# Kernel optimization log

Measured on AMD Instinct MI355X. Metric: run time of the kernel, lower is better.

Reference implementation:

```python
import jax, jax.numpy as jnp
import numpy as np

D_MODEL = 1024
NHEAD = 16
HEAD_DIM = D_MODEL // NHEAD


def setup_inputs() -> dict:
    key = jax.random.key(0)
    ks = jax.random.split(key, 11)
    B, S, D = 4, 2048, D_MODEL
    scale = 1.0 / np.sqrt(D)
    inp = {
        'q': jax.random.normal(ks[0], (B, S, D), jnp.float32),
        'k': jax.random.normal(ks[1], (B, S, D), jnp.float32),
        'v': jax.random.normal(ks[2], (B, S, D), jnp.float32),
        'Wq': jax.random.normal(ks[3], (D, D), jnp.float32) * scale,
        'bq': jnp.zeros((D,), jnp.float32),
        'Wk': jax.random.normal(ks[4], (D, D), jnp.float32) * scale,
        'bk': jnp.zeros((D,), jnp.float32),
        'Wv': jax.random.normal(ks[5], (D, D), jnp.float32) * scale,
        'bv': jnp.zeros((D,), jnp.float32),
        'Wo': jax.random.normal(ks[6], (D, D), jnp.float32) * scale,
        'bo': jnp.zeros((D,), jnp.float32),
    }
    return inp


def reference(q, k, v, Wq, bq, Wk, bk, Wv, bv, Wo, bo):
    B, S, D = q.shape
    H, Hd = NHEAD, HEAD_DIM
    # projections (torch Linear: x @ W.T + b), then split heads -> [B,H,S,Hd]
    qh = (q @ Wq.T + bq).reshape(B, S, H, Hd).transpose(0, 2, 1, 3)
    kh = (k @ Wk.T + bk).reshape(B, S, H, Hd).transpose(0, 2, 1, 3)
    vh = (v @ Wv.T + bv).reshape(B, S, H, Hd).transpose(0, 2, 1, 3)
    # scaled dot-product attention (mask=None, dropout eval-mode identity)
    scores = jnp.einsum('bhqd,bhkd->bhqk', qh, kh) / jnp.sqrt(jnp.float32(Hd))
    attn = jax.nn.softmax(scores, axis=-1)
    out = jnp.einsum('bhqk,bhkd->bhqd', attn, vh)  # [B,H,S,Hd]
    out = out.transpose(0, 2, 1, 3).reshape(B, S, D)
    return out @ Wo.T + bo
```

## Files before the change

### kernel.cpp

```cpp
#include <hip/hip_runtime.h>
#include <cstdint>

using u16 = unsigned short;
using u32 = unsigned int;
typedef __bf16 bf16x8 __attribute__((ext_vector_type(8)));
typedef float f32x4 __attribute__((ext_vector_type(4)));
typedef float f32x16 __attribute__((ext_vector_type(16)));
typedef u16 u16x8 __attribute__((ext_vector_type(8)));
typedef u16 u16x4 __attribute__((ext_vector_type(4)));

#define DEV static __device__ __forceinline__

DEV u16 f2bf(float f) {
  uint32_t u = __builtin_bit_cast(uint32_t, f);
  u += 0x7FFFu + ((u >> 16) & 1u);
  return (u16)(u >> 16);
}
DEV float bf2f(u16 h) {
  uint32_t u = ((uint32_t)h) << 16;
  return __builtin_bit_cast(float, u);
}
DEV u32 cvt_pk_bf16(float lo, float hi) {
  u32 r;
  asm("v_cvt_pk_bf16_f32 %0, %1, %2" : "=v"(r) : "v"(lo), "v"(hi));
  return r;
}

typedef const u32 __attribute__((address_space(1))) gcu32;
typedef u32 __attribute__((address_space(3))) lu32;
DEV void gl_lds16(const u16* g, u16* l) {
  __builtin_amdgcn_global_load_lds((gcu32*)g, (lu32*)l, 16, 0, 0);
}

#define MFMA(a, b, c) __builtin_amdgcn_mfma_f32_16x16x32_bf16((a), (b), (c), 0, 0, 0)
#define MFMA32(a, b, c) __builtin_amdgcn_mfma_f32_32x32x16_bf16((a), (b), (c), 0, 0, 0)

#define WAITV(n) asm volatile("s_waitcnt vmcnt(" #n ")" ::: "memory")

__global__ __launch_bounds__(256) void cvt_all(
    const float* __restrict__ q, const float* __restrict__ k,
    const float* __restrict__ v, const float* __restrict__ Wq,
    const float* __restrict__ Wk, const float* __restrict__ Wv,
    const float* __restrict__ Wo, u16* __restrict__ Xb, u16* __restrict__ Wb,
    u16* __restrict__ WoB) {
  const int bid = blockIdx.x;
  const float* src;
  u16* dst;
  size_t i;
  if (bid < 12288) {
    const int z = bid >> 12;
    src = (z == 0) ? q : (z == 1) ? k : v;
    dst = Xb + (size_t)z * 8388608;
    i = ((size_t)(bid & 4095) * 256 + threadIdx.x) * 8;
  } else {
    const int r = bid - 12288;
    const int z = r >> 9;
    src = (z == 0) ? Wq : (z == 1) ? Wk : (z == 2) ? Wv : Wo;
    dst = (z < 3) ? (Wb + (size_t)z * 1048576) : WoB;
    i = ((size_t)(r & 511) * 256 + threadIdx.x) * 8;
  }
  const float4 a = *(const float4*)(src + i);
  const float4 b = *(const float4*)(src + i + 4);
  u16x8 o;
  o[0] = f2bf(a.x); o[1] = f2bf(a.y); o[2] = f2bf(a.z); o[3] = f2bf(a.w);
  o[4] = f2bf(b.x); o[5] = f2bf(b.y); o[6] = f2bf(b.z); o[7] = f2bf(b.w);
  *(u16x8*)(dst + i) = o;
}

__global__ __launch_bounds__(256) void proj_gemm_bf(
    const u16* __restrict__ Xb, const u16* __restrict__ Wb,
    const float* __restrict__ bq, const float* __restrict__ bk,
    const float* __restrict__ bv, u16* __restrict__ Qh, u16* __restrict__ Kh,
    u16* __restrict__ Vt) {
  __shared__ u16 As[2][128 * 64];
  __shared__ u16 Bs[2][128 * 64];
  const int z = blockIdx.z;
  const int m0 = blockIdx.x * 128, n0 = blockIdx.y * 128;

  const u16* x = Xb + (size_t)z * 8388608;
  const u16* W = Wb + (size_t)z * 1048576;
  const float* bias = (z == 0) ? bq : (z == 1) ? bk : bv;
  u16* out = (z == 0) ? Qh : (z == 1) ? Kh : Vt;
  const float oscale = (z == 0) ? 0.18033688011112042f : 1.0f;

  const int tid = threadIdx.x;
  const int w = tid >> 6, lane = tid & 63;
  const int wr = w >> 1, wc = w & 1;
  const int lr = lane & 15, hq = lane >> 4;

  const int srow = w * 8 + (lane >> 3);
  const int scol = ((lane & 7) ^ ((lane >> 3) & 7)) * 8;
  const u16* xg = x + (size_t)(m0 + srow) * 1024 + scol;
  const u16* wg_ = W + (size_t)(n0 + srow) * 1024 + scol;

  f32x4 acc[4][4];
  const f32x4 fzero = {0.f, 0.f, 0.f, 0.f};
#pragma unroll
  for (int m = 0; m < 4; ++m)
#pragma unroll
    for (int n = 0; n < 4; ++n) acc[m][n] = fzero;

#define PSTAGE(b, t)                                                          \
  {                                                                           \
    _Pragma("unroll") for (int c = 0; c < 4; ++c) {                           \
      gl_lds16(xg + (size_t)c * 32 * 1024 + (t) * 64,                         \
               &As[b][c * 2048 + w * 512]);                                   \
      gl_lds16(wg_ + (size_t)c * 32 * 1024 + (t) * 64,                        \
               &Bs[b][c * 2048 + w * 512]);                                   \
    }                                                                         \
  }

  PSTAGE(0, 0);

#pragma unroll
  for (int t = 0; t < 16; ++t) {
    const int cur = t & 1;
    if (t < 15) {
      PSTAGE(cur ^ 1, t + 1);
      WAITV(8);
    } else {
      WAITV(0);
    }
    __builtin_amdgcn_s_barrier();
    __builtin_amdgcn_sched_barrier(0);
    __builtin_amdgcn_s_setprio(1);
#pragma unroll
    for (int kk = 0; kk < 2; ++kk) {
      bf16x8 a[4], b[4];
#pragma unroll
      for (int m = 0; m < 4; ++m) {
        const int row = wr * 64 + m * 16 + lr;
        a[m] = *(const bf16x8*)&As[cur][row * 64 + (((kk * 4 + hq) ^ (lr & 7)) * 8)];
      }
#pragma unroll
      for (int n = 0; n < 4; ++n) {
        const int row = wc * 64 + n * 16 + lr;
        b[n] = *(const bf16x8*)&Bs[cur][row * 64 + (((kk * 4 + hq) ^ (lr & 7)) * 8)];
      }
#pragma unroll
      for (int m = 0; m < 4; ++m)
#pragma unroll
        for (int n = 0; n < 4; ++n) acc[m][n] = MFMA(a[m], b[n], acc[m][n]);
    }
    __builtin_amdgcn_s_setprio(0);
    __builtin_amdgcn_sched_barrier(0);
    __builtin_amdgcn_s_barrier();
  }
#undef PSTAGE

#pragma unroll
  for (int n = 0; n < 4; ++n) {
    const int col = n0 + wc * 64 + n * 16 + lr;
    const float bvv = bias[col];
    const int h = col >> 6, d = col & 63;
#pragma unroll
    for (int m = 0; m < 4; ++m) {
#pragma unroll
      for (int j = 0; j < 4; ++j) {
        const int rowg = m0 + wr * 64 + m * 16 + hq * 4 + j;
        const int bb = rowg >> 11, s = rowg & 2047;
        const float val = (acc[m][n][j] + bvv) * oscale;
        size_t idx;
        if (z != 2)
          idx = ((size_t)(bb * 16 + h) * 2048 + s) * 64 + d;
        else
          idx = ((size_t)(bb * 16 + h) * 64 + d) * 2048 + s;
        out[idx] = f2bf(val);
      }
    }
  }
}

__global__ __launch_bounds__(256) void proj_gemm_f32(
    const float* __restrict__ q, const float* __restrict__ k,
    const float* __restrict__ v, const float* __restrict__ Wq,
    const float* __restrict__ Wk, const float* __restrict__ Wv,
    const float* __restrict__ bq, const float* __restrict__ bk,
    const float* __restrict__ bv, u16* __restrict__ Qh, u16* __restrict__ Kh,
    u16* __restrict__ Vt) {
  __shared__ u16 As[128][40];
  __shared__ u16 Bs[128][40];
  const int z = blockIdx.z;
  const float* x = (z == 0) ? q : (z == 1) ? k : v;
  const float* W = (z == 0) ? Wq : (z == 1) ? Wk : Wv;
  const float* bias = (z == 0) ? bq : (z == 1) ? bk : bv;
  u16* out = (z == 0) ? Qh : (z == 1) ? Kh : Vt;
  const float oscale = (z == 0) ? 0.18033688011112042f : 1.0f;

  const int tid = threadIdx.x;
  const int m0 = blockIdx.y * 128, n0 = blockIdx.x * 128;
  const int w = tid >> 6, lane = tid & 63;
  const int wr = w >> 1, wc = w & 1;
  const int lr = lane & 15, lk = (lane >> 4) * 8;
  const int srow = tid >> 3, sc4 = (tid & 7) * 4;

  f32x4 acc[4][4];
  const f32x4 fzero = {0.f, 0.f, 0.f, 0.f};
#pragma unroll
  for (int m = 0; m < 4; ++m)
#pragma unroll
    for (int n = 0; n < 4; ++n) acc[m][n] = fzero;

  for (int kt = 0; kt < 32; ++kt) {
    const int k0 = kt * 32;
    __syncthreads();
#pragma unroll
    for (int c = 0; c < 4; ++c) {
      const float4 av = *(const float4*)(x + (size_t)(m0 + c * 32 + srow) * 1024 + k0 + sc4);
      const float4 bvv = *(const float4*)(W + (size_t)(n0 + c * 32 + srow) * 1024 + k0 + sc4);
      u16x4 ah, bh;
      ah[0] = f2bf(av.x); ah[1] = f2bf(av.y); ah[2] = f2bf(av.z); ah[3] = f2bf(av.w);
      bh[0] = f2bf(bvv.x); bh[1] = f2bf(bvv.y); bh[2] = f2bf(bvv.z); bh[3] = f2bf(bvv.w);
      *(u16x4*)&As[c * 32 + srow][sc4] = ah;
      *(u16x4*)&Bs[c * 32 + srow][sc4] = bh;
    }
    __syncthreads();
    bf16x8 a[4], b[4];
#pragma unroll
    for (int m = 0; m < 4; ++m)
      a[m] = *(const bf16x8*)&As[wr * 64 + m * 16 + lr][lk];
#pragma unroll
    for (int n = 0; n < 4; ++n)
      b[n] = *(const bf16x8*)&Bs[wc * 64 + n * 16 + lr][lk];
#pragma unroll
    for (int m = 0; m < 4; ++m)
#pragma unroll
      for (int n = 0; n < 4; ++n) acc[m][n] = MFMA(a[m], b[n], acc[m][n]);
  }

#pragma unroll
  for (int n = 0; n < 4; ++n) {
    const int col = n0 + wc * 64 + n * 16 + lr;
    const float bvv = bias[col];
    const int h = col >> 6, d = col & 63;
#pragma unroll
    for (int m = 0; m < 4; ++m) {
#pragma unroll
      for (int j = 0; j < 4; ++j) {
        const int rowg = m0 + wr * 64 + m * 16 + (lane >> 4) * 4 + j;
        const int bb = rowg >> 11, s = rowg & 2047;
        const float val = (acc[m][n][j] + bvv) * oscale;
        size_t idx;
        if (z != 2)
          idx = ((size_t)(bb * 16 + h) * 2048 + s) * 64 + d;
        else
          idx = ((size_t)(bb * 16 + h) * 64 + d) * 2048 + s;
        out[idx] = f2bf(val);
      }
    }
  }
}

__global__ __launch_bounds__(512, 4) void attn_fwd(
    const u16* __restrict__ Qh, const u16* __restrict__ Kh,
    const u16* __restrict__ Vt, u16* __restrict__ Att) {
  __shared__ u16 Ks[128][72];
  __shared__ u16 Vs[64][136];
  const int tid = threadIdx.x;
  const int w = tid >> 6, lane = tid & 63;
  const int lq = lane & 31, h = lane >> 5;
  const int head = blockIdx.x, q0 = blockIdx.y * 256;
  const u16* Qb = Qh + (size_t)head * 131072;
  const u16* Kb = Kh + (size_t)head * 131072;
  const u16* Vb = Vt + (size_t)head * 131072;
  const int qrow = q0 + w * 32 + lq;

  bf16x8 qf[4];
#pragma unroll
  for (int dc = 0; dc < 4; ++dc)
    qf[dc] = *(const bf16x8*)(Qb + (size_t)qrow * 64 + dc * 16 + h * 8);

  f32x16 o0 = {}, o1 = {};
  float lsum = 0.f;

  const int srow = tid >> 3, scol = (tid & 7) * 8;
  uint4 kr0, kr1, vr0, vr1;
  kr0 = *(const uint4*)(Kb + (size_t)srow * 64 + scol);
  kr1 = *(const uint4*)(Kb + (size_t)(64 + srow) * 64 + scol);
  vr0 = *(const uint4*)(Vb + (size_t)srow * 2048 + scol);
  vr1 = *(const uint4*)(Vb + (size_t)srow * 2048 + 64 + scol);

  for (int kt = 0; kt < 16; ++kt) {
    __syncthreads();
    *(uint4*)&Ks[srow][scol] = kr0;
    *(uint4*)&Ks[64 + srow][scol] = kr1;
    *(uint4*)&Vs[srow][scol] = vr0;
    *(uint4*)&Vs[srow][64 + scol] = vr1;
    __syncthreads();
    if (kt + 1 < 16) {
      const int t0n = (kt + 1) * 128;
      kr0 = *(const uint4*)(Kb + (size_t)(t0n + srow) * 64 + scol);
      kr1 = *(const uint4*)(Kb + (size_t)(t0n + 64 + srow) * 64 + scol);
      vr0 = *(const uint4*)(Vb + (size_t)srow * 2048 + t0n + scol);
      vr1 = *(const uint4*)(Vb + (size_t)srow * 2048 + t0n + 64 + scol);
    }

#pragma unroll
    for (int half = 0; half < 2; ++half) {
      const int ko = half * 64;

      f32x16 s0 = {}, s1 = {};
      __builtin_amdgcn_s_setprio(1);
#pragma unroll
      for (int dc = 0; dc < 4; ++dc) {
        const bf16x8 k0 = *(const bf16x8*)&Ks[ko + lq][dc * 16 + h * 8];
        const bf16x8 k1 = *(const bf16x8*)&Ks[ko + 32 + lq][dc * 16 + h * 8];
        s0 = MFMA32(k0, qf[dc], s0);
        s1 = MFMA32(k1, qf[dc], s1);
      }
      __builtin_amdgcn_s_setprio(0);

      float rs = 0.f;
#pragma unroll
      for (int r = 0; r < 16; ++r) {
        s0[r] = __builtin_amdgcn_exp2f(s0[r]);
        s1[r] = __builtin_amdgcn_exp2f(s1[r]);
        rs += s0[r];
        rs += s1[r];
      }
      lsum += rs;

      u32 w0[8], w1[8];
#pragma unroll
      for (int b = 0; b < 4; ++b)
#pragma unroll
        for (int e = 0; e < 2; ++e) {
          w0[b * 2 + e] = cvt_pk_bf16(s0[4 * b + 2 * e], s0[4 * b + 2 * e + 1]);
          w1[b * 2 + e] = cvt_pk_bf16(s1[4 * b + 2 * e], s1[4 * b + 2 * e + 1]);
        }

      bf16x8 pa[4];
#pragma unroll
      for (int c = 0; c < 2; ++c) {
        u32 a0 = w0[(2 * c) * 2 + 0], b0 = w0[(2 * c + 1) * 2 + 0];
        u32 a1 = w0[(2 * c) * 2 + 1], b1 = w0[(2 * c + 1) * 2 + 1];
        asm("v_permlane32_swap_b32 %0, %1" : "+v"(a0), "+v"(b0));
        asm("v_permlane32_swap_b32 %0, %1" : "+v"(a1), "+v"(b1));
        const uint4 f = {a0, a1, b0, b1};
        pa[c] = __builtin_bit_cast(bf16x8, f);
      }
#pragma unroll
      for (int c = 0; c < 2; ++c) {
        u32 a0 = w1[(2 * c) * 2 + 0], b0 = w1[(2 * c + 1) * 2 + 0];
        u32 a1 = w1[(2 * c) * 2 + 1], b1 = w1[(2 * c + 1) * 2 + 1];
        asm("v_permlane32_swap_b32 %0, %1" : "+v"(a0), "+v"(b0));
        asm("v_permlane32_swap_b32 %0, %1" : "+v"(a1), "+v"(b1));
        const uint4 f = {a0, a1, b0, b1};
        pa[2 + c] = __builtin_bit_cast(bf16x8, f);
      }

      __builtin_amdgcn_s_setprio(1);
#pragma unroll
      for (int c = 0; c < 4; ++c) {
        const bf16x8 v0f = *(const bf16x8*)&Vs[lq][ko + c * 16 + h * 8];
        const bf16x8 v1f = *(const bf16x8*)&Vs[32 + lq][ko + c * 16 + h * 8];
        o0 = MFMA32(pa[c], v0f, o0);
        o1 = MFMA32(pa[c], v1f, o1);
      }
      __builtin_amdgcn_s_setprio(0);
    }
  }

  lsum += __shfl_xor(lsum, 32);

  const int bb = head >> 4, hh = head & 15;
  const float linv = 1.0f / lsum;
#pragma unroll
  for (int r = 0; r < 16; ++r) {
    const int qr = (r & 3) + 8 * (r >> 2) + 4 * h;
    const float li = __shfl(linv, qr);
    const int qg = q0 + w * 32 + qr;
    const size_t base = ((size_t)(bb * 2048 + qg)) * 1024 + hh * 64;
    Att[base + lq] = f2bf(o0[r] * li);
    Att[base + 32 + lq] = f2bf(o1[r] * li);
  }
}

__global__ __launch_bounds__(256) void out_gemm_bf(
    const u16* __restrict__ Att, const u16* __restrict__ WoB,
    const float* __restrict__ bo, float* __restrict__ out) {
  __shared__ u16 As[2][128 * 64];
  __shared__ u16 Bs[2][128 * 64];
  const int m0 = blockIdx.x * 128, n0 = blockIdx.y * 128;
  const int tid = threadIdx.x;
  const int w = tid >> 6, lane = tid & 63;
  const int wr = w >> 1, wc = w & 1;
  const int lr = lane & 15, hq = lane >> 4;

  const int srow = w * 8 + (lane >> 3);
  const int scol = ((lane & 7) ^ ((lane >> 3) & 7)) * 8;
  const u16* ag = Att + (size_t)(m0 + srow) * 1024 + scol;
  const u16* bg = WoB + (size_t)(n0 + srow) * 1024 + scol;

  f32x4 acc[4][4];
  const f32x4 fzero = {0.f, 0.f, 0.f, 0.f};
#pragma unroll
  for (int m = 0; m < 4; ++m)
#pragma unroll
    for (int n = 0; n < 4; ++n) acc[m][n] = fzero;

#define OSTAGE(b, t)                                                          \
  {                                                                           \
    _Pragma("unroll") for (int c = 0; c < 4; ++c) {                           \
      gl_lds16(ag + (size_t)c * 32 * 1024 + (t) * 64,                         \
               &As[b][c * 2048 + w * 512]);                                   \
      gl_lds16(bg + (size_t)c * 32 * 1024 + (t) * 64,                         \
               &Bs[b][c * 2048 + w * 512]);                                   \
    }                                                                         \
  }

  OSTAGE(0, 0);

#pragma unroll
  for (int t = 0; t < 16; ++t) {
    const int cur = t & 1;
    if (t < 15) {
      OSTAGE(cur ^ 1, t + 1);
      WAITV(8);
    } else {
      WAITV(0);
    }
    __builtin_amdgcn_s_barrier();
    __builtin_amdgcn_sched_barrier(0);
    __builtin_amdgcn_s_setprio(1);
#pragma unroll
    for (int kk = 0; kk < 2; ++kk) {
      bf16x8 a[4], b[4];
#pragma unroll
      for (int m = 0; m < 4; ++m) {
        const int row = wr * 64 + m * 16 + lr;
        a[m] = *(const bf16x8*)&As[cur][row * 64 + (((kk * 4 + hq) ^ (lr & 7)) * 8)];
      }
#pragma unroll
      for (int n = 0; n < 4; ++n) {
        const int row = wc * 64 + n * 16 + lr;
        b[n] = *(const bf16x8*)&Bs[cur][row * 64 + (((kk * 4 + hq) ^ (lr & 7)) * 8)];
      }
#pragma unroll
      for (int m = 0; m < 4; ++m)
#pragma unroll
        for (int n = 0; n < 4; ++n) acc[m][n] = MFMA(a[m], b[n], acc[m][n]);
    }
    __builtin_amdgcn_s_setprio(0);
    __builtin_amdgcn_sched_barrier(0);
    __builtin_amdgcn_s_barrier();
  }
#undef OSTAGE

#pragma unroll
  for (int n = 0; n < 4; ++n) {
    const int col = n0 + wc * 64 + n * 16 + lr;
    const float bvv = bo[col];
#pragma unroll
    for (int m = 0; m < 4; ++m)
#pragma unroll
      for (int j = 0; j < 4; ++j) {
        const int rowg = m0 + wr * 64 + m * 16 + hq * 4 + j;
        out[(size_t)rowg * 1024 + col] = acc[m][n][j] + bvv;
      }
  }
}

__global__ __launch_bounds__(256) void out_gemm_f32(
    const u16* __restrict__ Att, const float* __restrict__ Wo,
    const float* __restrict__ bo, float* __restrict__ out) {
  __shared__ u16 As[128][40], Bs[128][40];
  const int tid = threadIdx.x;
  const int m0 = blockIdx.y * 128, n0 = blockIdx.x * 128;
  const int w = tid >> 6, lane = tid & 63;
  const int wr = w >> 1, wc = w & 1;
  const int lr = lane & 15, lk = (lane >> 4) * 8;
  const int arow = tid >> 2, ac8 = (tid & 3) * 8;
  const int wrow = tid >> 3, wc4 = (tid & 7) * 4;

  f32x4 acc[4][4];
  const f32x4 fzero = {0.f, 0.f, 0.f, 0.f};
#pragma unroll
  for (int m = 0; m < 4; ++m)
#pragma unroll
    for (int n = 0; n < 4; ++n) acc[m][n] = fzero;

  for (int kt = 0; kt < 32; ++kt) {
    const int k0 = kt * 32;
    __syncthreads();
#pragma unroll
    for (int c = 0; c < 2; ++c) {
      *(uint4*)&As[c * 64 + arow][ac8] =
          *(const uint4*)(Att + (size_t)(m0 + c * 64 + arow) * 1024 + k0 + ac8);
    }
#pragma unroll
    for (int c = 0; c < 4; ++c) {
      const float4 wv = *(const float4*)(Wo + (size_t)(n0 + c * 32 + wrow) * 1024 + k0 + wc4);
      u16x4 hv;
      hv[0] = f2bf(wv.x); hv[1] = f2bf(wv.y); hv[2] = f2bf(wv.z); hv[3] = f2bf(wv.w);
      *(u16x4*)&Bs[c * 32 + wrow][wc4] = hv;
    }
    __syncthreads();
    bf16x8 a[4], b[4];
#pragma unroll
    for (int m = 0; m < 4; ++m)
      a[m] = *(const bf16x8*)&As[wr * 64 + m * 16 + lr][lk];
#pragma unroll
    for (int n = 0; n < 4; ++n)
      b[n] = *(const bf16x8*)&Bs[wc * 64 + n * 16 + lr][lk];
#pragma unroll
    for (int m = 0; m < 4; ++m)
#pragma unroll
      for (int n = 0; n < 4; ++n) acc[m][n] = MFMA(a[m], b[n], acc[m][n]);
  }

#pragma unroll
  for (int n = 0; n < 4; ++n) {
    const int col = n0 + wc * 64 + n * 16 + lr;
    const float bvv = bo[col];
#pragma unroll
    for (int m = 0; m < 4; ++m)
#pragma unroll
      for (int j = 0; j < 4; ++j) {
        const int rowg = m0 + wr * 64 + m * 16 + (lane >> 4) * 4 + j;
        out[(size_t)rowg * 1024 + col] = acc[m][n][j] + bvv;
      }
  }
}

extern "C" void kernel_launch(void* const* d_in, const int* in_sizes, int n_in,
                              void* d_out, int out_size, void* d_ws, size_t ws_size,
                              hipStream_t stream) {
  const float* q  = (const float*)d_in[0];
  const float* k  = (const float*)d_in[1];
  const float* v  = (const float*)d_in[2];
  const float* Wq = (const float*)d_in[3];
  const float* bq = (const float*)d_in[4];
  const float* Wk = (const float*)d_in[5];
  const float* bk = (const float*)d_in[6];
  const float* Wv = (const float*)d_in[7];
  const float* bv = (const float*)d_in[8];
  const float* Wo = (const float*)d_in[9];
  const float* bo = (const float*)d_in[10];

  u16* ws  = (u16*)d_ws;
  u16* Qh  = ws;
  u16* Kh  = ws + (size_t)8388608;
  u16* Vt  = ws + (size_t)16777216;
  u16* Att = ws + (size_t)25165824;
  u16* Xb  = ws + (size_t)25165824;
  u16* Wb  = ws + (size_t)50331648;
  u16* WoB = ws + (size_t)53477376;
  const size_t need = (size_t)55574528 * 2;

  if (ws_size >= need) {
    cvt_all<<<dim3(14336), dim3(256), 0, stream>>>(q, k, v, Wq, Wk, Wv, Wo, Xb,
                                                   Wb, WoB);
    proj_gemm_bf<<<dim3(64, 8, 3), dim3(256), 0, stream>>>(Xb, Wb, bq, bk, bv,
                                                           Qh, Kh, Vt);
    attn_fwd<<<dim3(64, 8), dim3(512), 0, stream>>>(Qh, Kh, Vt, Att);
    out_gemm_bf<<<dim3(64, 8), dim3(256), 0, stream>>>(Att, WoB, bo,
                                                       (float*)d_out);
  } else {
    proj_gemm_f32<<<dim3(8, 64, 3), dim3(256), 0, stream>>>(
        q, k, v, Wq, Wk, Wv, bq, bk, bv, Qh, Kh, Vt);
    attn_fwd<<<dim3(64, 8), dim3(512), 0, stream>>>(Qh, Kh, Vt, Att);
    out_gemm_f32<<<dim3(8, 64), dim3(256), 0, stream>>>(Att, Wo, bo,
                                                        (float*)d_out);
  }
}
```

Before: 191.3 us.

## Widen bf16 GEMM tiles to 128x256 with 8 waves and triple-buffered LDS

```diff
diff --git a/kernel.cpp b/kernel.cpp
--- a/kernel.cpp
+++ b/kernel.cpp
@@ -67,15 +67,15 @@
   *(u16x8*)(dst + i) = o;
 }
 
-__global__ __launch_bounds__(256) void proj_gemm_bf(
+__global__ __launch_bounds__(512, 2) void proj_gemm_bf(
     const u16* __restrict__ Xb, const u16* __restrict__ Wb,
     const float* __restrict__ bq, const float* __restrict__ bk,
     const float* __restrict__ bv, u16* __restrict__ Qh, u16* __restrict__ Kh,
     u16* __restrict__ Vt) {
-  __shared__ u16 As[2][128 * 64];
-  __shared__ u16 Bs[2][128 * 64];
+  __shared__ u16 As[3][128 * 64];
+  __shared__ u16 Bs[3][256 * 64];
   const int z = blockIdx.z;
-  const int m0 = blockIdx.x * 128, n0 = blockIdx.y * 128;
+  const int m0 = blockIdx.x * 128, n0 = blockIdx.y * 256;
 
   const u16* x = Xb + (size_t)z * 8388608;
   const u16* W = Wb + (size_t)z * 1048576;
@@ -85,13 +85,12 @@
 
   const int tid = threadIdx.x;
   const int w = tid >> 6, lane = tid & 63;
-  const int wr = w >> 1, wc = w & 1;
+  const int wr = w >> 2, wc = w & 3;
   const int lr = lane & 15, hq = lane >> 4;
 
-  const int srow = w * 8 + (lane >> 3);
   const int scol = ((lane & 7) ^ ((lane >> 3) & 7)) * 8;
-  const u16* xg = x + (size_t)(m0 + srow) * 1024 + scol;
-  const u16* wg_ = W + (size_t)(n0 + srow) * 1024 + scol;
+  const u16* xg = x + (size_t)(m0 + w * 8 + (lane >> 3)) * 1024 + scol;
+  const u16* wg_ = W + (size_t)(n0 + w * 8 + (lane >> 3)) * 1024 + scol;
 
   f32x4 acc[4][4];
   const f32x4 fzero = {0.f, 0.f, 0.f, 0.f};
@@ -102,22 +101,25 @@
 
 #define PSTAGE(b, t)                                                          \
   {                                                                           \
-    _Pragma("unroll") for (int c = 0; c < 4; ++c) {                           \
-      gl_lds16(xg + (size_t)c * 32 * 1024 + (t) * 64,                         \
-               &As[b][c * 2048 + w * 512]);                                   \
-      gl_lds16(wg_ + (size_t)c * 32 * 1024 + (t) * 64,                        \
-               &Bs[b][c * 2048 + w * 512]);                                   \
-    }                                                                         \
+    _Pragma("unroll") for (int l = 0; l < 2; ++l)                             \
+      gl_lds16(xg + (size_t)l * 64 * 1024 + (t) * 64,                         \
+               &As[b][(l * 512 + w * 64) * 8]);                               \
+    _Pragma("unroll") for (int l = 0; l < 4; ++l)                             \
+      gl_lds16(wg_ + (size_t)l * 64 * 1024 + (t) * 64,                        \
+               &Bs[b][(l * 512 + w * 64) * 8]);                               \
   }
 
   PSTAGE(0, 0);
+  PSTAGE(1, 1);
 
 #pragma unroll
   for (int t = 0; t < 16; ++t) {
-    const int cur = t & 1;
-    if (t < 15) {
-      PSTAGE(cur ^ 1, t + 1);
-      WAITV(8);
+    const int cur = t % 3;
+    if (t < 14) {
+      PSTAGE((t + 2) % 3, t + 2);
+      WAITV(12);
+    } else if (t == 14) {
+      WAITV(6);
     } else {
       WAITV(0);
     }
@@ -126,16 +128,17 @@
     __builtin_amdgcn_s_setprio(1);
 #pragma unroll
     for (int kk = 0; kk < 2; ++kk) {
+      const int rchunk = ((kk * 4 + hq) ^ (lr & 7)) * 8;
       bf16x8 a[4], b[4];
 #pragma unroll
       for (int m = 0; m < 4; ++m) {
         const int row = wr * 64 + m * 16 + lr;
-        a[m] = *(const bf16x8*)&As[cur][row * 64 + (((kk * 4 + hq) ^ (lr & 7)) * 8)];
+        a[m] = *(const bf16x8*)&As[cur][row * 64 + rchunk];
       }
 #pragma unroll
       for (int n = 0; n < 4; ++n) {
         const int row = wc * 64 + n * 16 + lr;
-        b[n] = *(const bf16x8*)&Bs[cur][row * 64 + (((kk * 4 + hq) ^ (lr & 7)) * 8)];
+        b[n] = *(const bf16x8*)&Bs[cur][row * 64 + rchunk];
       }
 #pragma unroll
       for (int m = 0; m < 4; ++m)
@@ -376,21 +379,20 @@
   }
 }
 
-__global__ __launch_bounds__(256) void out_gemm_bf(
+__global__ __launch_bounds__(512, 2) void out_gemm_bf(
     const u16* __restrict__ Att, const u16* __restrict__ WoB,
     const float* __restrict__ bo, float* __restrict__ out) {
-  __shared__ u16 As[2][128 * 64];
-  __shared__ u16 Bs[2][128 * 64];
-  const int m0 = blockIdx.x * 128, n0 = blockIdx.y * 128;
+  __shared__ u16 As[3][128 * 64];
+  __shared__ u16 Bs[3][256 * 64];
+  const int m0 = blockIdx.x * 128, n0 = blockIdx.y * 256;
   const int tid = threadIdx.x;
   const int w = tid >> 6, lane = tid & 63;
-  const int wr = w >> 1, wc = w & 1;
+  const int wr = w >> 2, wc = w & 3;
   const int lr = lane & 15, hq = lane >> 4;
 
-  const int srow = w * 8 + (lane >> 3);
   const int scol = ((lane & 7) ^ ((lane >> 3) & 7)) * 8;
-  const u16* ag = Att + (size_t)(m0 + srow) * 1024 + scol;
-  const u16* bg = WoB + (size_t)(n0 + srow) * 1024 + scol;
+  const u16* ag = Att + (size_t)(m0 + w * 8 + (lane >> 3)) * 1024 + scol;
+  const u16* bg = WoB + (size_t)(n0 + w * 8 + (lane >> 3)) * 1024 + scol;
 
   f32x4 acc[4][4];
   const f32x4 fzero = {0.f, 0.f, 0.f, 0.f};
@@ -401,22 +403,25 @@
 
 #define OSTAGE(b, t)                                                          \
   {                                                                           \
-    _Pragma("unroll") for (int c = 0; c < 4; ++c) {                           \
-      gl_lds16(ag + (size_t)c * 32 * 1024 + (t) * 64,                         \
-               &As[b][c * 2048 + w * 512]);                                   \
-      gl_lds16(bg + (size_t)c * 32 * 1024 + (t) * 64,                         \
-               &Bs[b][c * 2048 + w * 512]);                                   \
-    }                                                                         \
+    _Pragma("unroll") for (int l = 0; l < 2; ++l)                             \
+      gl_lds16(ag + (size_t)l * 64 * 1024 + (t) * 64,                         \
+               &As[b][(l * 512 + w * 64) * 8]);                               \
+    _Pragma("unroll") for (int l = 0; l < 4; ++l)                             \
+      gl_lds16(bg + (size_t)l * 64 * 1024 + (t) * 64,                         \
+               &Bs[b][(l * 512 + w * 64) * 8]);                               \
   }
 
   OSTAGE(0, 0);
+  OSTAGE(1, 1);
 
 #pragma unroll
   for (int t = 0; t < 16; ++t) {
-    const int cur = t & 1;
-    if (t < 15) {
-      OSTAGE(cur ^ 1, t + 1);
-      WAITV(8);
+    const int cur = t % 3;
+    if (t < 14) {
+      OSTAGE((t + 2) % 3, t + 2);
+      WAITV(12);
+    } else if (t == 14) {
+      WAITV(6);
     } else {
       WAITV(0);
     }
@@ -425,16 +430,17 @@
     __builtin_amdgcn_s_setprio(1);
 #pragma unroll
     for (int kk = 0; kk < 2; ++kk) {
+      const int rchunk = ((kk * 4 + hq) ^ (lr & 7)) * 8;
       bf16x8 a[4], b[4];
 #pragma unroll
       for (int m = 0; m < 4; ++m) {
         const int row = wr * 64 + m * 16 + lr;
-        a[m] = *(const bf16x8*)&As[cur][row * 64 + (((kk * 4 + hq) ^ (lr & 7)) * 8)];
+        a[m] = *(const bf16x8*)&As[cur][row * 64 + rchunk];
       }
 #pragma unroll
       for (int n = 0; n < 4; ++n) {
         const int row = wc * 64 + n * 16 + lr;
-        b[n] = *(const bf16x8*)&Bs[cur][row * 64 + (((kk * 4 + hq) ^ (lr & 7)) * 8)];
+        b[n] = *(const bf16x8*)&Bs[cur][row * 64 + rchunk];
       }
 #pragma unroll
       for (int m = 0; m < 4; ++m)
@@ -551,10 +557,10 @@
   if (ws_size >= need) {
     cvt_all<<<dim3(14336), dim3(256), 0, stream>>>(q, k, v, Wq, Wk, Wv, Wo, Xb,
                                                    Wb, WoB);
-    proj_gemm_bf<<<dim3(64, 8, 3), dim3(256), 0, stream>>>(Xb, Wb, bq, bk, bv,
+    proj_gemm_bf<<<dim3(64, 4, 3), dim3(512), 0, stream>>>(Xb, Wb, bq, bk, bv,
                                                            Qh, Kh, Vt);
     attn_fwd<<<dim3(64, 8), dim3(512), 0, stream>>>(Qh, Kh, Vt, Att);
-    out_gemm_bf<<<dim3(64, 8), dim3(256), 0, stream>>>(Att, WoB, bo,
+    out_gemm_bf<<<dim3(64, 4), dim3(512), 0, stream>>>(Att, WoB, bo,
                                                        (float*)d_out);
   } else {
     proj_gemm_f32<<<dim3(8, 64, 3), dim3(256), 0, stream>>>(
```

New measurement: 195.5 us. 1.02x slower.

## Enlarge projection GEMM tiles to 256x256 with 8 waves and interleaved B loads

Applied to the files above, without the earlier changes.

```diff
diff --git a/kernel.cpp b/kernel.cpp
--- a/kernel.cpp
+++ b/kernel.cpp
@@ -67,15 +67,15 @@
   *(u16x8*)(dst + i) = o;
 }
 
-__global__ __launch_bounds__(256) void proj_gemm_bf(
+__global__ __launch_bounds__(512, 2) void proj_gemm_bf(
     const u16* __restrict__ Xb, const u16* __restrict__ Wb,
     const float* __restrict__ bq, const float* __restrict__ bk,
     const float* __restrict__ bv, u16* __restrict__ Qh, u16* __restrict__ Kh,
     u16* __restrict__ Vt) {
-  __shared__ u16 As[2][128 * 64];
-  __shared__ u16 Bs[2][128 * 64];
+  __shared__ u16 As[2][256 * 64];
+  __shared__ u16 Bs[2][256 * 64];
   const int z = blockIdx.z;
-  const int m0 = blockIdx.x * 128, n0 = blockIdx.y * 128;
+  const int m0 = blockIdx.x * 256, n0 = blockIdx.y * 256;
 
   const u16* x = Xb + (size_t)z * 8388608;
   const u16* W = Wb + (size_t)z * 1048576;
@@ -85,34 +85,34 @@
 
   const int tid = threadIdx.x;
   const int w = tid >> 6, lane = tid & 63;
-  const int wr = w >> 1, wc = w & 1;
+  const int wr = w >> 2, wc = w & 3;
   const int lr = lane & 15, hq = lane >> 4;
 
-  const int srow = w * 8 + (lane >> 3);
   const int scol = ((lane & 7) ^ ((lane >> 3) & 7)) * 8;
-  const u16* xg = x + (size_t)(m0 + srow) * 1024 + scol;
-  const u16* wg_ = W + (size_t)(n0 + srow) * 1024 + scol;
-
-  f32x4 acc[4][4];
+  const u16* xg = x + (size_t)(m0 + w * 8 + (lane >> 3)) * 1024 + scol;
+  const u16* wg_ = W + (size_t)(n0 + w * 8 + (lane >> 3)) * 1024 + scol;
+
+  f32x4 acc[8][4];
   const f32x4 fzero = {0.f, 0.f, 0.f, 0.f};
 #pragma unroll
-  for (int m = 0; m < 4; ++m)
+  for (int m = 0; m < 8; ++m)
 #pragma unroll
     for (int n = 0; n < 4; ++n) acc[m][n] = fzero;
 
 #define PSTAGE(b, t)                                                          \
   {                                                                           \
-    _Pragma("unroll") for (int c = 0; c < 4; ++c) {                           \
-      gl_lds16(xg + (size_t)c * 32 * 1024 + (t) * 64,                         \
-               &As[b][c * 2048 + w * 512]);                                   \
-      gl_lds16(wg_ + (size_t)c * 32 * 1024 + (t) * 64,                        \
-               &Bs[b][c * 2048 + w * 512]);                                   \
-    }                                                                         \
-  }
+    _Pragma("unroll") for (int l = 0; l < 4; ++l)                             \
+      gl_lds16(xg + (size_t)l * 64 * 1024 + (t) * 64,                         \
+               &As[b][(l * 64 + w * 8) * 64]);                                \
+    _Pragma("unroll") for (int l = 0; l < 4; ++l)                             \
+      gl_lds16(wg_ + (size_t)l * 64 * 1024 + (t) * 64,                        \
+               &Bs[b][(l * 64 + w * 8) * 64]);                                \
+  }
+#define RCH(kk) ((((kk) * 4 + hq) ^ (lr & 7)) * 8)
 
   PSTAGE(0, 0);
 
-#pragma unroll
+#pragma unroll 1
   for (int t = 0; t < 16; ++t) {
     const int cur = t & 1;
     if (t < 15) {
@@ -122,31 +122,47 @@
       WAITV(0);
     }
     __builtin_amdgcn_s_barrier();
-    __builtin_amdgcn_sched_barrier(0);
-    __builtin_amdgcn_s_setprio(1);
+
+    bf16x8 a[8];
 #pragma unroll
     for (int kk = 0; kk < 2; ++kk) {
-      bf16x8 a[4], b[4];
-#pragma unroll
-      for (int m = 0; m < 4; ++m) {
-        const int row = wr * 64 + m * 16 + lr;
-        a[m] = *(const bf16x8*)&As[cur][row * 64 + (((kk * 4 + hq) ^ (lr & 7)) * 8)];
-      }
-#pragma unroll
-      for (int n = 0; n < 4; ++n) {
-        const int row = wc * 64 + n * 16 + lr;
-        b[n] = *(const bf16x8*)&Bs[cur][row * 64 + (((kk * 4 + hq) ^ (lr & 7)) * 8)];
-      }
-#pragma unroll
-      for (int m = 0; m < 4; ++m)
-#pragma unroll
-        for (int n = 0; n < 4; ++n) acc[m][n] = MFMA(a[m], b[n], acc[m][n]);
-    }
-    __builtin_amdgcn_s_setprio(0);
-    __builtin_amdgcn_sched_barrier(0);
-    __builtin_amdgcn_s_barrier();
+#pragma unroll
+      for (int m = 0; m < 8; ++m)
+        a[m] = *(const bf16x8*)&As[cur][(wr * 128 + m * 16 + lr) * 64 + RCH(kk)];
+      {
+        const bf16x8 b0 =
+            *(const bf16x8*)&Bs[cur][(wc * 64 + 0 * 16 + lr) * 64 + RCH(kk)];
+        const bf16x8 b1 =
+            *(const bf16x8*)&Bs[cur][(wc * 64 + 1 * 16 + lr) * 64 + RCH(kk)];
+        __builtin_amdgcn_s_barrier();
+        __builtin_amdgcn_s_setprio(1);
+#pragma unroll
+        for (int m = 0; m < 8; ++m) {
+          acc[m][0] = MFMA(a[m], b0, acc[m][0]);
+          acc[m][1] = MFMA(a[m], b1, acc[m][1]);
+        }
+        __builtin_amdgcn_s_setprio(0);
+        __builtin_amdgcn_s_barrier();
+      }
+      {
+        const bf16x8 b2 =
+            *(const bf16x8*)&Bs[cur][(wc * 64 + 2 * 16 + lr) * 64 + RCH(kk)];
+        const bf16x8 b3 =
+            *(const bf16x8*)&Bs[cur][(wc * 64 + 3 * 16 + lr) * 64 + RCH(kk)];
+        __builtin_amdgcn_s_barrier();
+        __builtin_amdgcn_s_setprio(1);
+#pragma unroll
+        for (int m = 0; m < 8; ++m) {
+          acc[m][2] = MFMA(a[m], b2, acc[m][2]);
+          acc[m][3] = MFMA(a[m], b3, acc[m][3]);
+        }
+        __builtin_amdgcn_s_setprio(0);
+        __builtin_amdgcn_s_barrier();
+      }
+    }
   }
 #undef PSTAGE
+#undef RCH
 
 #pragma unroll
   for (int n = 0; n < 4; ++n) {
@@ -154,10 +170,10 @@
     const float bvv = bias[col];
     const int h = col >> 6, d = col & 63;
 #pragma unroll
-    for (int m = 0; m < 4; ++m) {
+    for (int m = 0; m < 8; ++m) {
 #pragma unroll
       for (int j = 0; j < 4; ++j) {
-        const int rowg = m0 + wr * 64 + m * 16 + hq * 4 + j;
+        const int rowg = m0 + wr * 128 + m * 16 + hq * 4 + j;
         const int bb = rowg >> 11, s = rowg & 2047;
         const float val = (acc[m][n][j] + bvv) * oscale;
         size_t idx;
@@ -551,7 +567,7 @@
   if (ws_size >= need) {
     cvt_all<<<dim3(14336), dim3(256), 0, stream>>>(q, k, v, Wq, Wk, Wv, Wo, Xb,
                                                    Wb, WoB);
-    proj_gemm_bf<<<dim3(64, 8, 3), dim3(256), 0, stream>>>(Xb, Wb, bq, bk, bv,
+    proj_gemm_bf<<<dim3(32, 4, 3), dim3(512), 0, stream>>>(Xb, Wb, bq, bk, bv,
                                                            Qh, Kh, Vt);
     attn_fwd<<<dim3(64, 8), dim3(512), 0, stream>>>(Qh, Kh, Vt, Att);
     out_gemm_bf<<<dim3(64, 8), dim3(256), 0, stream>>>(Att, WoB, bo,
```

After: 230.2 us. 1.2x slower.
